# Optimization experiments

Measured on AMD Instinct MI355X. Metric: run time of the kernel, lower is better.

## Reference

```python
import jax, jax.numpy as jnp
import numpy as np

D = 2048
H = 16
DH = D // H  # 128
B = 512
EPS = 1e-5


def _layernorm(x, g, b):
    m = jnp.mean(x, axis=-1, keepdims=True)
    v = jnp.mean((x - m) ** 2, axis=-1, keepdims=True)
    return (x - m) * jax.lax.rsqrt(v + EPS) * g + b


def setup_inputs() -> dict:
    key = jax.random.key(0)
    ks = jax.random.split(key, 16)
    s_in = 1.0 / np.sqrt(D)
    s_ff = 1.0 / np.sqrt(4 * D)
    return {
        "x": jax.random.normal(ks[0], (B, D), jnp.float32),
        # per-head q/k/v projections, stacked over heads: [H, D, DH]
        "Wq": jax.random.uniform(ks[1], (H, D, DH), jnp.float32, -s_in, s_in),
        "bq": jax.random.uniform(ks[2], (H, DH), jnp.float32, -s_in, s_in),
        "Wk": jax.random.uniform(ks[3], (H, D, DH), jnp.float32, -s_in, s_in),
        "bk": jax.random.uniform(ks[4], (H, DH), jnp.float32, -s_in, s_in),
        "Wv": jax.random.uniform(ks[5], (H, D, DH), jnp.float32, -s_in, s_in),
        "bv": jax.random.uniform(ks[6], (H, DH), jnp.float32, -s_in, s_in),
        "Wo": jax.random.uniform(ks[7], (D, D), jnp.float32, -s_in, s_in),
        "bo": jax.random.uniform(ks[8], (D,), jnp.float32, -s_in, s_in),
        "W1": jax.random.uniform(ks[9], (D, 4 * D), jnp.float32, -s_in, s_in),
        "b1": jax.random.uniform(ks[10], (4 * D,), jnp.float32, -s_in, s_in),
        "W2": jax.random.uniform(ks[11], (4 * D, D), jnp.float32, -s_ff, s_ff),
        "b2": jax.random.uniform(ks[12], (D,), jnp.float32, -s_ff, s_ff),
        "g1": jnp.ones((D,), jnp.float32),
        "be1": jnp.zeros((D,), jnp.float32),
        "g2": jnp.ones((D,), jnp.float32),
        "be2": jnp.zeros((D,), jnp.float32),
    }


def reference(x, Wq, bq, Wk, bk, Wv, bv, Wo, bo, W1, b1, W2, b2, g1, be1, g2, be2):
    # --- pre-norm attention branch ---
    h = _layernorm(x, g1, be1)                       # [B, D]
    q = jnp.einsum('bd,hde->bhe', h, Wq) + bq        # [B, H, DH]
    k = jnp.einsum('bd,hde->bhe', h, Wk) + bk
    v = jnp.einsum('bd,hde->bhe', h, Wv) + bv
    # outer-product 'attention' per sample: [B, H, DH, DH]
    attn = q[..., :, None] * k[..., None, :] / jnp.sqrt(jnp.float32(DH))
    attn = jax.nn.softmax(attn, axis=-1)
    o = jnp.einsum('bhij,bhj->bhi', attn, v)         # [B, H, DH]
    o = o.reshape(x.shape[0], H * DH)                # concat over heads
    x = x + o @ Wo + bo
    # --- pre-norm FFN branch ---
    h2 = _layernorm(x, g2, be2)
    x = x + jax.nn.relu(h2 @ W1 + b1) @ W2 + b2
    return x
```

## Files before the change

kernel.cpp:

```cpp
#include <hip/hip_runtime.h>
#include <hip/hip_bf16.h>
#include <math.h>


#define DDIM 2048
#define HHEADS 16
#define DHEAD 128
#define BROWS 512
#define LN_EPS 1e-5f

typedef __bf16 bf16x8_t __attribute__((ext_vector_type(8)));
typedef __bf16 bf16x4_t __attribute__((ext_vector_type(4)));
typedef __bf16 bf16x2_t __attribute__((ext_vector_type(2)));
typedef float f32x4_t __attribute__((ext_vector_type(4)));

#define GLD16(gptr, lptr)                                                     \
    __builtin_amdgcn_global_load_lds(                                         \
        (const __attribute__((address_space(1))) void*)(gptr),                \
        (__attribute__((address_space(3))) void*)(lptr), 16, 0, 0)

__global__ __launch_bounds__(256) void ln_kernel(const float* __restrict__ x,
                                                 const float* __restrict__ g,
                                                 const float* __restrict__ b,
                                                 __bf16* __restrict__ out) {
    const int row = blockIdx.x;
    const int tid = threadIdx.x;
    const float4* x4 = (const float4*)(x + (size_t)row * DDIM);
    float4 a = x4[2 * tid];
    float4 c = x4[2 * tid + 1];
    float s  = a.x + a.y + a.z + a.w + c.x + c.y + c.z + c.w;
    float s2 = a.x*a.x + a.y*a.y + a.z*a.z + a.w*a.w
             + c.x*c.x + c.y*c.y + c.z*c.z + c.w*c.w;
    #pragma unroll
    for (int off = 32; off > 0; off >>= 1) {
        s  += __shfl_down(s, off);
        s2 += __shfl_down(s2, off);
    }
    __shared__ float ps[4], ps2[4];
    __shared__ float mean_s, rstd_s;
    const int lane = tid & 63, w = tid >> 6;
    if (lane == 0) { ps[w] = s; ps2[w] = s2; }
    __syncthreads();
    if (tid == 0) {
        float S  = ps[0] + ps[1] + ps[2] + ps[3];
        float S2 = ps2[0] + ps2[1] + ps2[2] + ps2[3];
        float m  = S * (1.0f / DDIM);
        float var = S2 * (1.0f / DDIM) - m * m;
        mean_s = m;
        rstd_s = rsqrtf(var + LN_EPS);
    }
    __syncthreads();
    const float m = mean_s, r = rstd_s;
    const float4* g4 = (const float4*)g;
    const float4* b4 = (const float4*)b;
    float4 ga = g4[2 * tid], gb = g4[2 * tid + 1];
    float4 ba = b4[2 * tid], bb = b4[2 * tid + 1];
    bf16x8_t o;
    o[0] = (__bf16)((a.x - m) * r * ga.x + ba.x);
    o[1] = (__bf16)((a.y - m) * r * ga.y + ba.y);
    o[2] = (__bf16)((a.z - m) * r * ga.z + ba.z);
    o[3] = (__bf16)((a.w - m) * r * ga.w + ba.w);
    o[4] = (__bf16)((c.x - m) * r * gb.x + bb.x);
    o[5] = (__bf16)((c.y - m) * r * gb.y + bb.y);
    o[6] = (__bf16)((c.z - m) * r * gb.z + bb.z);
    o[7] = (__bf16)((c.w - m) * r * gb.w + bb.w);
    *(bf16x8_t*)(out + (size_t)row * DDIM + tid * 8) = o;
}

template <int TM, int TN, int SPLITZ, int OUT_BF16, int RELU, int RES, int QKV>
__global__ __launch_bounds__(512, 4) void gemm_af(
    const __bf16* __restrict__ A, int K,
    const float* __restrict__ Bq, const float* __restrict__ Bk,
    const float* __restrict__ Bv, int ldb,
    const float* __restrict__ bias, const float* __restrict__ biasB,
    const float* __restrict__ biasC, const float* __restrict__ Res,
    void* __restrict__ Cout, int N) {
    constexpr int DEPTH = 3;
    constexpr int STG = (TM + TN) * 64;
    __shared__ __align__(16) __bf16 smem[DEPTH * STG];

    const int tid = threadIdx.x;
    const int w = tid >> 6, lane = tid & 63;

    const int gx = gridDim.x, gy = gridDim.y, gz = gridDim.z;
    int l = blockIdx.x + gx * (blockIdx.y + gy * blockIdx.z);
    const int xcd = l & 7;
    int i0 = l >> 3;
    const int by = i0 % gy; i0 /= gy;
    const int bz = i0 % gz; i0 /= gz;
    const int bx = xcd * (gx >> 3) + i0;

    const int m0 = by * TM, n0 = bx * TN;
    const int Kloc = K / SPLITZ;
    const int kb = bz * Kloc;
    const int NK = Kloc / 64;

    constexpr int LA = TM / 64;
    const int srow = lane >> 3;
    const int sslot = (lane & 7) ^ srow;
    const __bf16* srcs[LA];
    int toff[LA];
    #pragma unroll
    for (int i = 0; i < LA; i++) {
        const int t = w + 8 * i;
        toff[i] = t * 512;
        srcs[i] = A + (size_t)(m0 + t * 8 + srow) * K + kb + sslot * 8;
    }

    constexpr int KPER = TN / 32;
    constexpr int LB = KPER;
    constexpr int NPR = TN / 4;
    const int np = tid & (NPR - 1);
    const int kp = tid / NPR;
    const int k0 = kp * KPER, n0t = np * 4;

    const float* bbase;
    if (QKV) {
        const int seg = n0 >> 11;
        const float* sel = (seg == 0) ? Bq : (seg == 1) ? Bk : Bv;
        bbase = sel + (size_t)((n0 & 2047) >> 7) * (DDIM * DHEAD);
    } else {
        bbase = Bq + n0;
    }
    const float* bthr = bbase + (size_t)(kb + k0) * ldb + n0t;
    const size_t bstep = (size_t)64 * ldb;

    int bwoff[4];
    {
        const int bslot = k0 >> 3, bhalf = (k0 & 7) * 2;
        #pragma unroll
        for (int j = 0; j < 4; j++) {
            const int n = n0t + j;
            const int fb = (n ^ (n >> 2)) & 7;
            bwoff[j] = (TM + n) * 128 + ((bslot ^ fb) * 16) + bhalf;
        }
    }

    constexpr int MI = TM / 32, NJ = TN / 32;
    const int wg = w & 3, kh = w >> 2;
    const int wm = (wg >> 1) * (TM / 2), wn = (wg & 1) * (TN / 2);
    const int fm = lane & 15, quad = lane >> 4;
    const int slq = kh * 4 + quad;
    int aoff[MI], boff[NJ];
    #pragma unroll
    for (int i = 0; i < MI; i++)
        aoff[i] = (wm + 16 * i + fm) * 128 + ((slq ^ (fm & 7)) * 16);
    #pragma unroll
    for (int j = 0; j < NJ; j++) {
        const int n = wn + 16 * j + fm;
        const int fb = (n ^ (n >> 2)) & 7;
        boff[j] = (TM + n) * 128 + ((slq ^ fb) * 16);
    }

    f32x4_t acc[MI][NJ] = {};
    f32x4_t bufA[KPER], bufB[KPER];

    auto loadB = [&](int ks2, f32x4_t (&dst)[KPER]) {
        const float* q = bthr + (size_t)ks2 * bstep;
        #pragma unroll
        for (int j = 0; j < KPER; j++)
            dst[j] = *(const f32x4_t*)(q + (size_t)j * ldb);
    };
    auto writeB = [&](int slot, const f32x4_t (&src)[KPER]) {
        char* stg = (char*)smem + slot * (STG * 2);
        #pragma unroll
        for (int j = 0; j < 4; j++) {
            if constexpr (KPER == 4) {
                bf16x4_t u;
                u[0] = (__bf16)src[0][j]; u[1] = (__bf16)src[1][j];
                u[2] = (__bf16)src[2][j]; u[3] = (__bf16)src[3][j];
                *(bf16x4_t*)(stg + bwoff[j]) = u;
            } else {
                bf16x2_t u;
                u[0] = (__bf16)src[0][j]; u[1] = (__bf16)src[1][j];
                *(bf16x2_t*)(stg + bwoff[j]) = u;
            }
        }
    };

    loadB(0, bufA);
    loadB(1, bufB);
    #pragma unroll
    for (int i = 0; i < LA; i++) GLD16(srcs[i], smem + toff[i]);
    writeB(0, bufA);
    loadB(2, bufA);
    #pragma unroll
    for (int i = 0; i < LA; i++) GLD16(srcs[i] + 64, smem + STG + toff[i]);

    auto body = [&](int ks, f32x4_t (&buf)[KPER]) {
        if (ks < NK - 2)
            asm volatile("s_waitcnt vmcnt(%0) lgkmcnt(0)\n\ts_barrier"
                         :: "i"(LB + LA) : "memory");
        else
            asm volatile("s_waitcnt vmcnt(0) lgkmcnt(0)\n\ts_barrier"
                         ::: "memory");
        if (ks + 1 < NK) writeB((ks + 1) % DEPTH, buf);
        if (ks + 3 < NK) loadB(ks + 3, buf);
        if (ks + 2 < NK) {
            #pragma unroll
            for (int i = 0; i < LA; i++)
                GLD16(srcs[i] + (size_t)(ks + 2) * 64,
                      smem + ((ks + 2) % DEPTH) * STG + toff[i]);
        }
        const char* st = (const char*)smem + (ks % DEPTH) * (STG * 2);
        bf16x8_t a[MI], b[NJ];
        #pragma unroll
        for (int i = 0; i < MI; i++) a[i] = *(const bf16x8_t*)(st + aoff[i]);
        #pragma unroll
        for (int j = 0; j < NJ; j++) b[j] = *(const bf16x8_t*)(st + boff[j]);
        __builtin_amdgcn_s_setprio(1);
        #pragma unroll
        for (int i = 0; i < MI; i++)
            #pragma unroll
            for (int j = 0; j < NJ; j++)
                acc[i][j] = __builtin_amdgcn_mfma_f32_16x16x32_bf16(
                    a[i], b[j], acc[i][j], 0, 0, 0);
        __builtin_amdgcn_s_setprio(0);
    };

    for (int ks = 0; ks < NK; ks += 2) {
        body(ks, bufB);
        body(ks + 1, bufA);
    }

    char* mrg = (char*)smem + wg * (MI * NJ * 64 * 16);
    __syncthreads();
    if (kh == 1) {
        #pragma unroll
        for (int i = 0; i < MI; i++)
            #pragma unroll
            for (int j = 0; j < NJ; j++)
                *(f32x4_t*)(mrg + (((i * NJ + j) * 64) + lane) * 16) = acc[i][j];
    }
    __syncthreads();
    if (kh == 1) return;
    #pragma unroll
    for (int i = 0; i < MI; i++)
        #pragma unroll
        for (int j = 0; j < NJ; j++) {
            const f32x4_t p =
                *(const f32x4_t*)(mrg + (((i * NJ + j) * 64) + lane) * 16);
            acc[i][j][0] += p[0]; acc[i][j][1] += p[1];
            acc[i][j][2] += p[2]; acc[i][j][3] += p[3];
        }

    if (SPLITZ > 1) {
        float* P = (float*)Cout + (size_t)bz * (gy * TM) * N;
        #pragma unroll
        for (int i = 0; i < MI; i++)
            #pragma unroll
            for (int j = 0; j < NJ; j++) {
                const int col = n0 + wn + 16 * j + fm;
                #pragma unroll
                for (int r = 0; r < 4; r++) {
                    const int row = m0 + wm + 16 * i + quad * 4 + r;
                    P[(size_t)row * N + col] = acc[i][j][r];
                }
            }
    } else {
        const float* bp = bias;
        if (QKV) {
            const int seg = n0 >> 11;
            bp = (seg == 0) ? bias : (seg == 1) ? biasB : biasC;
        }
        #pragma unroll
        for (int i = 0; i < MI; i++)
            #pragma unroll
            for (int j = 0; j < NJ; j++) {
                const int col = n0 + wn + 16 * j + fm;
                const float bcol = QKV ? bp[col & 2047] : bp[col];
                #pragma unroll
                for (int r = 0; r < 4; r++) {
                    const int row = m0 + wm + 16 * i + quad * 4 + r;
                    float val = acc[i][j][r] + bcol;
                    if (RES) val += Res[(size_t)row * N + col];
                    if (RELU) val = fmaxf(val, 0.0f);
                    if (OUT_BF16)
                        ((__bf16*)Cout)[(size_t)row * N + col] = (__bf16)val;
                    else
                        ((float*)Cout)[(size_t)row * N + col] = val;
                }
            }
    }
}

template <int NS>
__global__ __launch_bounds__(256) void reduce_splitk(
    const float* __restrict__ part, const float* __restrict__ Res,
    const float* __restrict__ bias, float* __restrict__ out) {
    const int idx = blockIdx.x * 256 + threadIdx.x;
    const float4 b4 = ((const float4*)bias)[idx & 511];
    float4 r = ((const float4*)Res)[idx];
    #pragma unroll
    for (int s = 0; s < NS; s++) {
        const float4 p = ((const float4*)part)[(size_t)s * 262144 + idx];
        r.x += p.x; r.y += p.y; r.z += p.z; r.w += p.w;
    }
    r.x += b4.x; r.y += b4.y; r.z += b4.z; r.w += b4.w;
    ((float4*)out)[idx] = r;
}

__global__ __launch_bounds__(128) void attn_kernel(
    const __bf16* __restrict__ qkv, __bf16* __restrict__ o) {
    const int bh = blockIdx.x;
    const int b = bh >> 4, h = bh & 15;
    const size_t base = (size_t)b * (3 * DDIM) + h * DHEAD;
    const int tid = threadIdx.x;
    __shared__ float ks[DHEAD], vs[DHEAD];
    ks[tid] = (float)qkv[base + DDIM + tid];
    vs[tid] = (float)qkv[base + 2 * DDIM + tid];
    __syncthreads();
    const float a = (float)qkv[base + tid] * 0.08838834764831845f;
    float den = 0.0f, num = 0.0f;
    #pragma unroll 8
    for (int j = 0; j < DHEAD; j++) {
        float e = __expf(a * ks[j]);
        den += e;
        num += e * vs[j];
    }
    o[(size_t)b * DDIM + h * DHEAD + tid] = (__bf16)(num / den);
}

extern "C" void kernel_launch(void* const* d_in, const int* in_sizes, int n_in,
                              void* d_out, int out_size, void* d_ws, size_t ws_size,
                              hipStream_t stream) {
    const float* x   = (const float*)d_in[0];
    const float* Wq  = (const float*)d_in[1];
    const float* bq  = (const float*)d_in[2];
    const float* Wk  = (const float*)d_in[3];
    const float* bk  = (const float*)d_in[4];
    const float* Wv  = (const float*)d_in[5];
    const float* bv  = (const float*)d_in[6];
    const float* Wo  = (const float*)d_in[7];
    const float* bo  = (const float*)d_in[8];
    const float* W1  = (const float*)d_in[9];
    const float* b1  = (const float*)d_in[10];
    const float* W2  = (const float*)d_in[11];
    const float* b2  = (const float*)d_in[12];
    const float* g1  = (const float*)d_in[13];
    const float* be1 = (const float*)d_in[14];
    const float* g2  = (const float*)d_in[15];
    const float* be2 = (const float*)d_in[16];
    float* out = (float*)d_out;

    char* base = (char*)d_ws;
    __bf16* h   = (__bf16*)(base + 0);
    __bf16* qkv = (__bf16*)(base + 2097152);
    __bf16* ob  = (__bf16*)(base + 8388608);
    float*  x1  = (float*)(base + 10485760);
    __bf16* h2  = (__bf16*)(base + 14680064);
    __bf16* t   = (__bf16*)(base + 16777216);
    float*  w2P = (float*)(base + 25165824);

    ln_kernel<<<BROWS, 256, 0, stream>>>(x, g1, be1, h);

    gemm_af<64, 128, 1, 1, 0, 0, 1><<<dim3(48, 8), 512, 0, stream>>>(
        h, DDIM, Wq, Wk, Wv, DHEAD, bq, bk, bv, nullptr, qkv, 3 * DDIM);

    attn_kernel<<<BROWS * HHEADS, 128, 0, stream>>>(qkv, ob);

    gemm_af<64, 64, 1, 0, 0, 1, 0><<<dim3(32, 8), 512, 0, stream>>>(
        ob, DDIM, Wo, nullptr, nullptr, DDIM, bo, nullptr, nullptr, x,
        x1, DDIM);

    ln_kernel<<<BROWS, 256, 0, stream>>>(x1, g2, be2, h2);

    gemm_af<64, 128, 1, 1, 1, 0, 0><<<dim3(64, 8), 512, 0, stream>>>(
        h2, DDIM, W1, nullptr, nullptr, 4 * DDIM, b1, nullptr, nullptr,
        nullptr, t, 4 * DDIM);

    gemm_af<64, 128, 4, 0, 0, 0, 0><<<dim3(16, 8, 4), 512, 0, stream>>>(
        t, 4 * DDIM, W2, nullptr, nullptr, DDIM, nullptr, nullptr, nullptr,
        nullptr, w2P, DDIM);

    reduce_splitk<4><<<1024, 256, 0, stream>>>(w2P, x1, b2, out);
}
```

Baseline: 389.8 us.

## Pre-cast all weights to bf16 in a fused cast+LN kernel, drop split-K for W2

Adds a kernel that converts every fp32 weight matrix to bf16 in a workspace, fused with the first layernorm. The GEMMs then stream bf16 weights instead of fp32, and the W2 GEMM runs without split-K, fusing bias and residual directly and removing the reduction kernel. The extra cast pass reads all fp32 weights once and writes bf16 copies every call, so total weight traffic per call rises rather than falls. The W2 GEMM also now iterates the full K=8192 per block with fewer blocks.

```diff
diff --git a/kernel.cpp b/kernel.cpp
--- a/kernel.cpp
+++ b/kernel.cpp
@@ -67,11 +67,88 @@
     *(bf16x8_t*)(out + (size_t)row * DDIM + tid * 8) = o;
 }
 
-template <int TM, int TN, int SPLITZ, int OUT_BF16, int RELU, int RES, int QKV>
+__global__ __launch_bounds__(256) void cast_ln_kernel(
+    const float* __restrict__ Wq, const float* __restrict__ Wk,
+    const float* __restrict__ Wv, const float* __restrict__ Wo,
+    const float* __restrict__ W1, const float* __restrict__ W2,
+    const float* __restrict__ x, const float* __restrict__ g1,
+    const float* __restrict__ be1,
+    __bf16* __restrict__ wc, __bf16* __restrict__ h) {
+    __shared__ float sh[32];
+    const int bid = blockIdx.x;
+    const int tid = threadIdx.x;
+    if (bid < 12288) {
+        const int seg = bid >> 10;
+        const float* src;
+        if (seg == 0) src = Wq;
+        else if (seg == 1) src = Wk;
+        else if (seg == 2) src = Wv;
+        else if (seg == 3) src = Wo;
+        else if (seg < 8) src = W1 + (size_t)(seg - 4) * 4194304;
+        else src = W2 + (size_t)(seg - 8) * 4194304;
+        __bf16* dst = wc + (size_t)seg * 4194304;
+        const size_t i = (size_t)(bid & 1023) * 4096 + (size_t)tid * 16;
+        const float4* s4 = (const float4*)(src + i);
+        const float4 v0 = s4[0], v1 = s4[1], v2 = s4[2], v3 = s4[3];
+        bf16x8_t o0, o1;
+        o0[0] = (__bf16)v0.x; o0[1] = (__bf16)v0.y;
+        o0[2] = (__bf16)v0.z; o0[3] = (__bf16)v0.w;
+        o0[4] = (__bf16)v1.x; o0[5] = (__bf16)v1.y;
+        o0[6] = (__bf16)v1.z; o0[7] = (__bf16)v1.w;
+        o1[0] = (__bf16)v2.x; o1[1] = (__bf16)v2.y;
+        o1[2] = (__bf16)v2.z; o1[3] = (__bf16)v2.w;
+        o1[4] = (__bf16)v3.x; o1[5] = (__bf16)v3.y;
+        o1[6] = (__bf16)v3.z; o1[7] = (__bf16)v3.w;
+        *(bf16x8_t*)(dst + i) = o0;
+        *(bf16x8_t*)(dst + i + 8) = o1;
+    } else {
+        const int row = bid - 12288;
+        const float4* x4 = (const float4*)(x + (size_t)row * DDIM);
+        float4 a = x4[2 * tid];
+        float4 c = x4[2 * tid + 1];
+        float s  = a.x + a.y + a.z + a.w + c.x + c.y + c.z + c.w;
+        float s2 = a.x*a.x + a.y*a.y + a.z*a.z + a.w*a.w
+                 + c.x*c.x + c.y*c.y + c.z*c.z + c.w*c.w;
+        #pragma unroll
+        for (int off = 32; off > 0; off >>= 1) {
+            s  += __shfl_down(s, off);
+            s2 += __shfl_down(s2, off);
+        }
+        const int lane = tid & 63, w = tid >> 6;
+        if (lane == 0) { sh[w] = s; sh[8 + w] = s2; }
+        __syncthreads();
+        if (tid == 0) {
+            float S  = sh[0] + sh[1] + sh[2] + sh[3];
+            float S2 = sh[8] + sh[9] + sh[10] + sh[11];
+            float m  = S * (1.0f / DDIM);
+            float var = S2 * (1.0f / DDIM) - m * m;
+            sh[16] = m;
+            sh[17] = rsqrtf(var + LN_EPS);
+        }
+        __syncthreads();
+        const float m = sh[16], r = sh[17];
+        const float4* g4 = (const float4*)g1;
+        const float4* b4 = (const float4*)be1;
+        float4 ga = g4[2 * tid], gb = g4[2 * tid + 1];
+        float4 ba = b4[2 * tid], bb = b4[2 * tid + 1];
+        bf16x8_t o;
+        o[0] = (__bf16)((a.x - m) * r * ga.x + ba.x);
+        o[1] = (__bf16)((a.y - m) * r * ga.y + ba.y);
+        o[2] = (__bf16)((a.z - m) * r * ga.z + ba.z);
+        o[3] = (__bf16)((a.w - m) * r * ga.w + ba.w);
+        o[4] = (__bf16)((c.x - m) * r * gb.x + bb.x);
+        o[5] = (__bf16)((c.y - m) * r * gb.y + bb.y);
+        o[6] = (__bf16)((c.z - m) * r * gb.z + bb.z);
+        o[7] = (__bf16)((c.w - m) * r * gb.w + bb.w);
+        *(bf16x8_t*)(h + (size_t)row * DDIM + tid * 8) = o;
+    }
+}
+
+template <int TM, int TN, int OUT_BF16, int RELU, int RES, int QKV>
 __global__ __launch_bounds__(512, 4) void gemm_af(
     const __bf16* __restrict__ A, int K,
-    const float* __restrict__ Bq, const float* __restrict__ Bk,
-    const float* __restrict__ Bv, int ldb,
+    const __bf16* __restrict__ Bq, const __bf16* __restrict__ Bk,
+    const __bf16* __restrict__ Bv, int ldb,
     const float* __restrict__ bias, const float* __restrict__ biasB,
     const float* __restrict__ biasC, const float* __restrict__ Res,
     void* __restrict__ Cout, int N) {
@@ -82,18 +159,15 @@
     const int tid = threadIdx.x;
     const int w = tid >> 6, lane = tid & 63;
 
-    const int gx = gridDim.x, gy = gridDim.y, gz = gridDim.z;
-    int l = blockIdx.x + gx * (blockIdx.y + gy * blockIdx.z);
+    const int gx = gridDim.x, gy = gridDim.y;
+    int l = blockIdx.x + gx * blockIdx.y;
     const int xcd = l & 7;
     int i0 = l >> 3;
     const int by = i0 % gy; i0 /= gy;
-    const int bz = i0 % gz; i0 /= gz;
     const int bx = xcd * (gx >> 3) + i0;
 
     const int m0 = by * TM, n0 = bx * TN;
-    const int Kloc = K / SPLITZ;
-    const int kb = bz * Kloc;
-    const int NK = Kloc / 64;
+    const int NK = K / 64;
 
     constexpr int LA = TM / 64;
     const int srow = lane >> 3;
@@ -104,7 +178,7 @@
     for (int i = 0; i < LA; i++) {
         const int t = w + 8 * i;
         toff[i] = t * 512;
-        srcs[i] = A + (size_t)(m0 + t * 8 + srow) * K + kb + sslot * 8;
+        srcs[i] = A + (size_t)(m0 + t * 8 + srow) * K + sslot * 8;
     }
 
     constexpr int KPER = TN / 32;
@@ -114,15 +188,15 @@
     const int kp = tid / NPR;
     const int k0 = kp * KPER, n0t = np * 4;
 
-    const float* bbase;
+    const __bf16* bbase;
     if (QKV) {
         const int seg = n0 >> 11;
-        const float* sel = (seg == 0) ? Bq : (seg == 1) ? Bk : Bv;
+        const __bf16* sel = (seg == 0) ? Bq : (seg == 1) ? Bk : Bv;
         bbase = sel + (size_t)((n0 & 2047) >> 7) * (DDIM * DHEAD);
     } else {
         bbase = Bq + n0;
     }
-    const float* bthr = bbase + (size_t)(kb + k0) * ldb + n0t;
+    const __bf16* bthr = bbase + (size_t)k0 * ldb + n0t;
     const size_t bstep = (size_t)64 * ldb;
 
     int bwoff[4];
@@ -153,26 +227,26 @@
     }
 
     f32x4_t acc[MI][NJ] = {};
-    f32x4_t bufA[KPER], bufB[KPER];
-
-    auto loadB = [&](int ks2, f32x4_t (&dst)[KPER]) {
-        const float* q = bthr + (size_t)ks2 * bstep;
+    bf16x4_t bufA[KPER], bufB[KPER];
+
+    auto loadB = [&](int ks2, bf16x4_t (&dst)[KPER]) {
+        const __bf16* q = bthr + (size_t)ks2 * bstep;
         #pragma unroll
         for (int j = 0; j < KPER; j++)
-            dst[j] = *(const f32x4_t*)(q + (size_t)j * ldb);
+            dst[j] = *(const bf16x4_t*)(q + (size_t)j * ldb);
     };
-    auto writeB = [&](int slot, const f32x4_t (&src)[KPER]) {
+    auto writeB = [&](int slot, const bf16x4_t (&src)[KPER]) {
         char* stg = (char*)smem + slot * (STG * 2);
         #pragma unroll
         for (int j = 0; j < 4; j++) {
             if constexpr (KPER == 4) {
                 bf16x4_t u;
-                u[0] = (__bf16)src[0][j]; u[1] = (__bf16)src[1][j];
-                u[2] = (__bf16)src[2][j]; u[3] = (__bf16)src[3][j];
+                u[0] = src[0][j]; u[1] = src[1][j];
+                u[2] = src[2][j]; u[3] = src[3][j];
                 *(bf16x4_t*)(stg + bwoff[j]) = u;
             } else {
                 bf16x2_t u;
-                u[0] = (__bf16)src[0][j]; u[1] = (__bf16)src[1][j];
+                u[0] = src[0][j]; u[1] = src[1][j];
                 *(bf16x2_t*)(stg + bwoff[j]) = u;
             }
         }
@@ -187,7 +261,7 @@
     #pragma unroll
     for (int i = 0; i < LA; i++) GLD16(srcs[i] + 64, smem + STG + toff[i]);
 
-    auto body = [&](int ks, f32x4_t (&buf)[KPER]) {
+    auto body = [&](int ks, bf16x4_t (&buf)[KPER]) {
         if (ks < NK - 2)
             asm volatile("s_waitcnt vmcnt(%0) lgkmcnt(0)\n\ts_barrier"
                          :: "i"(LB + LA) : "memory");
@@ -244,60 +318,29 @@
             acc[i][j][2] += p[2]; acc[i][j][3] += p[3];
         }
 
-    if (SPLITZ > 1) {
-        float* P = (float*)Cout + (size_t)bz * (gy * TM) * N;
-        #pragma unroll
-        for (int i = 0; i < MI; i++)
+    const float* bp = bias;
+    if (QKV) {
+        const int seg = n0 >> 11;
+        bp = (seg == 0) ? bias : (seg == 1) ? biasB : biasC;
+    }
+    #pragma unroll
+    for (int i = 0; i < MI; i++)
+        #pragma unroll
+        for (int j = 0; j < NJ; j++) {
+            const int col = n0 + wn + 16 * j + fm;
+            const float bcol = QKV ? bp[col & 2047] : bp[col];
             #pragma unroll
-            for (int j = 0; j < NJ; j++) {
-                const int col = n0 + wn + 16 * j + fm;
-                #pragma unroll
-                for (int r = 0; r < 4; r++) {
-                    const int row = m0 + wm + 16 * i + quad * 4 + r;
-                    P[(size_t)row * N + col] = acc[i][j][r];
-                }
+            for (int r = 0; r < 4; r++) {
+                const int row = m0 + wm + 16 * i + quad * 4 + r;
+                float val = acc[i][j][r] + bcol;
+                if (RES) val += Res[(size_t)row * N + col];
+                if (RELU) val = fmaxf(val, 0.0f);
+                if (OUT_BF16)
+                    ((__bf16*)Cout)[(size_t)row * N + col] = (__bf16)val;
+                else
+                    ((float*)Cout)[(size_t)row * N + col] = val;
             }
-    } else {
-        const float* bp = bias;
-        if (QKV) {
-            const int seg = n0 >> 11;
-            bp = (seg == 0) ? bias : (seg == 1) ? biasB : biasC;
-        }
-        #pragma unroll
-        for (int i = 0; i < MI; i++)
-            #pragma unroll
-            for (int j = 0; j < NJ; j++) {
-                const int col = n0 + wn + 16 * j + fm;
-                const float bcol = QKV ? bp[col & 2047] : bp[col];
-                #pragma unroll
-                for (int r = 0; r < 4; r++) {
-                    const int row = m0 + wm + 16 * i + quad * 4 + r;
-                    float val = acc[i][j][r] + bcol;
-                    if (RES) val += Res[(size_t)row * N + col];
-                    if (RELU) val = fmaxf(val, 0.0f);
-                    if (OUT_BF16)
-                        ((__bf16*)Cout)[(size_t)row * N + col] = (__bf16)val;
-                    else
-                        ((float*)Cout)[(size_t)row * N + col] = val;
-                }
-            }
-    }
-}
-
-template <int NS>
-__global__ __launch_bounds__(256) void reduce_splitk(
-    const float* __restrict__ part, const float* __restrict__ Res,
-    const float* __restrict__ bias, float* __restrict__ out) {
-    const int idx = blockIdx.x * 256 + threadIdx.x;
-    const float4 b4 = ((const float4*)bias)[idx & 511];
-    float4 r = ((const float4*)Res)[idx];
-    #pragma unroll
-    for (int s = 0; s < NS; s++) {
-        const float4 p = ((const float4*)part)[(size_t)s * 262144 + idx];
-        r.x += p.x; r.y += p.y; r.z += p.z; r.w += p.w;
-    }
-    r.x += b4.x; r.y += b4.y; r.z += b4.z; r.w += b4.w;
-    ((float4*)out)[idx] = r;
+        }
 }
 
 __global__ __launch_bounds__(128) void attn_kernel(
@@ -344,34 +387,40 @@
     float* out = (float*)d_out;
 
     char* base = (char*)d_ws;
-    __bf16* h   = (__bf16*)(base + 0);
-    __bf16* qkv = (__bf16*)(base + 2097152);
-    __bf16* ob  = (__bf16*)(base + 8388608);
-    float*  x1  = (float*)(base + 10485760);
-    __bf16* h2  = (__bf16*)(base + 14680064);
-    __bf16* t   = (__bf16*)(base + 16777216);
-    float*  w2P = (float*)(base + 25165824);
-
-    ln_kernel<<<BROWS, 256, 0, stream>>>(x, g1, be1, h);
-
-    gemm_af<64, 128, 1, 1, 0, 0, 1><<<dim3(48, 8), 512, 0, stream>>>(
-        h, DDIM, Wq, Wk, Wv, DHEAD, bq, bk, bv, nullptr, qkv, 3 * DDIM);
+    __bf16* wc   = (__bf16*)(base + 0);
+    __bf16* Wq_c = wc;
+    __bf16* Wk_c = wc + 4194304;
+    __bf16* Wv_c = wc + 2 * 4194304;
+    __bf16* Wo_c = wc + 3 * 4194304;
+    __bf16* W1_c = wc + 4 * 4194304;
+    __bf16* W2_c = wc + 8 * 4194304;
+    char* act = base + 100663296;
+    __bf16* h   = (__bf16*)(act + 0);
+    __bf16* qkv = (__bf16*)(act + 2097152);
+    __bf16* ob  = (__bf16*)(act + 8388608);
+    float*  x1  = (float*)(act + 10485760);
+    __bf16* h2  = (__bf16*)(act + 14680064);
+    __bf16* t   = (__bf16*)(act + 16777216);
+
+    cast_ln_kernel<<<12800, 256, 0, stream>>>(Wq, Wk, Wv, Wo, W1, W2, x, g1,
+                                              be1, wc, h);
+
+    gemm_af<64, 128, 1, 0, 0, 1><<<dim3(48, 8), 512, 0, stream>>>(
+        h, DDIM, Wq_c, Wk_c, Wv_c, DHEAD, bq, bk, bv, nullptr, qkv, 3 * DDIM);
 
     attn_kernel<<<BROWS * HHEADS, 128, 0, stream>>>(qkv, ob);
 
-    gemm_af<64, 64, 1, 0, 0, 1, 0><<<dim3(32, 8), 512, 0, stream>>>(
-        ob, DDIM, Wo, nullptr, nullptr, DDIM, bo, nullptr, nullptr, x,
+    gemm_af<64, 64, 0, 0, 1, 0><<<dim3(32, 8), 512, 0, stream>>>(
+        ob, DDIM, Wo_c, nullptr, nullptr, DDIM, bo, nullptr, nullptr, x,
         x1, DDIM);
 
     ln_kernel<<<BROWS, 256, 0, stream>>>(x1, g2, be2, h2);
 
-    gemm_af<64, 128, 1, 1, 1, 0, 0><<<dim3(64, 8), 512, 0, stream>>>(
-        h2, DDIM, W1, nullptr, nullptr, 4 * DDIM, b1, nullptr, nullptr,
+    gemm_af<64, 128, 1, 1, 0, 0><<<dim3(64, 8), 512, 0, stream>>>(
+        h2, DDIM, W1_c, nullptr, nullptr, 4 * DDIM, b1, nullptr, nullptr,
         nullptr, t, 4 * DDIM);
 
-    gemm_af<64, 128, 4, 0, 0, 0, 0><<<dim3(16, 8, 4), 512, 0, stream>>>(
-        t, 4 * DDIM, W2, nullptr, nullptr, DDIM, nullptr, nullptr, nullptr,
-        nullptr, w2P, DDIM);
-
-    reduce_splitk<4><<<1024, 256, 0, stream>>>(w2P, x1, b2, out);
+    gemm_af<64, 64, 0, 0, 1, 0><<<dim3(32, 8), 512, 0, stream>>>(
+        t, 4 * DDIM, W2_c, nullptr, nullptr, DDIM, b2, nullptr, nullptr, x1,
+        out, DDIM);
 }
```

After: 397.2 us. No clear change (+1.9%).

## Use 128x128 GEMM tiles, split-K the Wo projection, fuse reduce with LayerNorm

Applied to the files above, without the earlier changes.

Fixes all GEMMs at 128x128 tiles with four 4x4 MFMA fragments per wave and lowers the occupancy hint to 2, halving the M-direction grid. This raises reuse of the fp32 weight tiles that each block converts to bf16. The Wo projection now runs as a 4-way split-K GEMM writing partial sums. A new kernel adds those partials, the residual and the bias, then applies the second LayerNorm in one pass, replacing the separate LN launch. The cost is fewer blocks per GEMM (192–256 on a large GPU), more registers and LDS per block, and extra partial-sum traffic for Wo.

```diff
diff --git a/kernel.cpp b/kernel.cpp
--- a/kernel.cpp
+++ b/kernel.cpp
@@ -11,7 +11,6 @@
 
 typedef __bf16 bf16x8_t __attribute__((ext_vector_type(8)));
 typedef __bf16 bf16x4_t __attribute__((ext_vector_type(4)));
-typedef __bf16 bf16x2_t __attribute__((ext_vector_type(2)));
 typedef float f32x4_t __attribute__((ext_vector_type(4)));
 
 #define GLD16(gptr, lptr)                                                     \
@@ -67,15 +66,15 @@
     *(bf16x8_t*)(out + (size_t)row * DDIM + tid * 8) = o;
 }
 
-template <int TM, int TN, int SPLITZ, int OUT_BF16, int RELU, int RES, int QKV>
-__global__ __launch_bounds__(512, 4) void gemm_af(
+template <int SPLITZ, int OUT_BF16, int RELU, int RES, int QKV>
+__global__ __launch_bounds__(512, 2) void gemm_af(
     const __bf16* __restrict__ A, int K,
     const float* __restrict__ Bq, const float* __restrict__ Bk,
     const float* __restrict__ Bv, int ldb,
     const float* __restrict__ bias, const float* __restrict__ biasB,
     const float* __restrict__ biasC, const float* __restrict__ Res,
     void* __restrict__ Cout, int N) {
-    constexpr int DEPTH = 3;
+    constexpr int TM = 128, TN = 128, DEPTH = 3;
     constexpr int STG = (TM + TN) * 64;
     __shared__ __align__(16) __bf16 smem[DEPTH * STG];
 
@@ -107,7 +106,7 @@
         srcs[i] = A + (size_t)(m0 + t * 8 + srow) * K + kb + sslot * 8;
     }
 
-    constexpr int KPER = TN / 32;
+    constexpr int KPER = 4;
     constexpr int LB = KPER;
     constexpr int NPR = TN / 4;
     const int np = tid & (NPR - 1);
@@ -136,9 +135,9 @@
         }
     }
 
-    constexpr int MI = TM / 32, NJ = TN / 32;
+    constexpr int MI = 4, NJ = 4;
     const int wg = w & 3, kh = w >> 2;
-    const int wm = (wg >> 1) * (TM / 2), wn = (wg & 1) * (TN / 2);
+    const int wm = (wg >> 1) * 64, wn = (wg & 1) * 64;
     const int fm = lane & 15, quad = lane >> 4;
     const int slq = kh * 4 + quad;
     int aoff[MI], boff[NJ];
@@ -165,16 +164,10 @@
         char* stg = (char*)smem + slot * (STG * 2);
         #pragma unroll
         for (int j = 0; j < 4; j++) {
-            if constexpr (KPER == 4) {
-                bf16x4_t u;
-                u[0] = (__bf16)src[0][j]; u[1] = (__bf16)src[1][j];
-                u[2] = (__bf16)src[2][j]; u[3] = (__bf16)src[3][j];
-                *(bf16x4_t*)(stg + bwoff[j]) = u;
-            } else {
-                bf16x2_t u;
-                u[0] = (__bf16)src[0][j]; u[1] = (__bf16)src[1][j];
-                *(bf16x2_t*)(stg + bwoff[j]) = u;
-            }
+            bf16x4_t u;
+            u[0] = (__bf16)src[0][j]; u[1] = (__bf16)src[1][j];
+            u[2] = (__bf16)src[2][j]; u[3] = (__bf16)src[3][j];
+            *(bf16x4_t*)(stg + bwoff[j]) = u;
         }
     };
 
@@ -223,7 +216,7 @@
         body(ks + 1, bufA);
     }
 
-    char* mrg = (char*)smem + wg * (MI * NJ * 64 * 16);
+    char* mrg = (char*)smem + wg * 16384;
     __syncthreads();
     if (kh == 1) {
         #pragma unroll
@@ -298,6 +291,71 @@
     }
     r.x += b4.x; r.y += b4.y; r.z += b4.z; r.w += b4.w;
     ((float4*)out)[idx] = r;
+}
+
+template <int NS>
+__global__ __launch_bounds__(256) void reduce_ln_kernel(
+    const float* __restrict__ part, const float* __restrict__ x,
+    const float* __restrict__ bo, const float* __restrict__ g,
+    const float* __restrict__ be, float* __restrict__ x1,
+    __bf16* __restrict__ h2) {
+    const int row = blockIdx.x;
+    const int tid = threadIdx.x;
+    const size_t rbase = (size_t)row * DDIM;
+    float v[8];
+    #pragma unroll
+    for (int p = 0; p < 2; p++) {
+        const int c = tid * 8 + p * 4;
+        float4 r = *(const float4*)(x + rbase + c);
+        const float4 b4 = *(const float4*)(bo + c);
+        r.x += b4.x; r.y += b4.y; r.z += b4.z; r.w += b4.w;
+        #pragma unroll
+        for (int s = 0; s < NS; s++) {
+            const float4 q =
+                *(const float4*)(part + (size_t)s * BROWS * DDIM + rbase + c);
+            r.x += q.x; r.y += q.y; r.z += q.z; r.w += q.w;
+        }
+        *(float4*)(x1 + rbase + c) = r;
+        v[p * 4 + 0] = r.x; v[p * 4 + 1] = r.y;
+        v[p * 4 + 2] = r.z; v[p * 4 + 3] = r.w;
+    }
+    float s = 0.f, s2 = 0.f;
+    #pragma unroll
+    for (int i = 0; i < 8; i++) { s += v[i]; s2 += v[i] * v[i]; }
+    #pragma unroll
+    for (int off = 32; off > 0; off >>= 1) {
+        s  += __shfl_down(s, off);
+        s2 += __shfl_down(s2, off);
+    }
+    __shared__ float ps[4], ps2[4];
+    __shared__ float mean_s, rstd_s;
+    const int lane = tid & 63, wv = tid >> 6;
+    if (lane == 0) { ps[wv] = s; ps2[wv] = s2; }
+    __syncthreads();
+    if (tid == 0) {
+        float S  = ps[0] + ps[1] + ps[2] + ps[3];
+        float S2 = ps2[0] + ps2[1] + ps2[2] + ps2[3];
+        float m  = S * (1.0f / DDIM);
+        float var = S2 * (1.0f / DDIM) - m * m;
+        mean_s = m;
+        rstd_s = rsqrtf(var + LN_EPS);
+    }
+    __syncthreads();
+    const float m = mean_s, r = rstd_s;
+    const float4* g4 = (const float4*)g;
+    const float4* b4 = (const float4*)be;
+    float4 ga = g4[2 * tid], gb = g4[2 * tid + 1];
+    float4 ba = b4[2 * tid], bb = b4[2 * tid + 1];
+    bf16x8_t o;
+    o[0] = (__bf16)((v[0] - m) * r * ga.x + ba.x);
+    o[1] = (__bf16)((v[1] - m) * r * ga.y + ba.y);
+    o[2] = (__bf16)((v[2] - m) * r * ga.z + ba.z);
+    o[3] = (__bf16)((v[3] - m) * r * ga.w + ba.w);
+    o[4] = (__bf16)((v[4] - m) * r * gb.x + bb.x);
+    o[5] = (__bf16)((v[5] - m) * r * gb.y + bb.y);
+    o[6] = (__bf16)((v[6] - m) * r * gb.z + bb.z);
+    o[7] = (__bf16)((v[7] - m) * r * gb.w + bb.w);
+    *(bf16x8_t*)(h2 + rbase + tid * 8) = o;
 }
 
 __global__ __launch_bounds__(128) void attn_kernel(
@@ -343,33 +401,34 @@
     const float* be2 = (const float*)d_in[16];
     float* out = (float*)d_out;
 
-    char* base = (char*)d_ws;
-    __bf16* h   = (__bf16*)(base + 0);
-    __bf16* qkv = (__bf16*)(base + 2097152);
-    __bf16* ob  = (__bf16*)(base + 8388608);
-    float*  x1  = (float*)(base + 10485760);
-    __bf16* h2  = (__bf16*)(base + 14680064);
-    __bf16* t   = (__bf16*)(base + 16777216);
-    float*  w2P = (float*)(base + 25165824);
+    char* act = (char*)d_ws;
+    __bf16* h   = (__bf16*)(act + 0);
+    __bf16* qkv = (__bf16*)(act + 2097152);
+    __bf16* ob  = (__bf16*)(act + 8388608);
+    float*  x1  = (float*)(act + 10485760);
+    __bf16* h2  = (__bf16*)(act + 14680064);
+    __bf16* t   = (__bf16*)(act + 16777216);
+    float*  woP = (float*)(act + 25165824);
+    float*  w2P = (float*)(act + 41943040);
 
     ln_kernel<<<BROWS, 256, 0, stream>>>(x, g1, be1, h);
 
-    gemm_af<64, 128, 1, 1, 0, 0, 1><<<dim3(48, 8), 512, 0, stream>>>(
+    gemm_af<1, 1, 0, 0, 1><<<dim3(48, 4), 512, 0, stream>>>(
         h, DDIM, Wq, Wk, Wv, DHEAD, bq, bk, bv, nullptr, qkv, 3 * DDIM);
 
     attn_kernel<<<BROWS * HHEADS, 128, 0, stream>>>(qkv, ob);
 
-    gemm_af<64, 64, 1, 0, 0, 1, 0><<<dim3(32, 8), 512, 0, stream>>>(
-        ob, DDIM, Wo, nullptr, nullptr, DDIM, bo, nullptr, nullptr, x,
-        x1, DDIM);
-
-    ln_kernel<<<BROWS, 256, 0, stream>>>(x1, g2, be2, h2);
-
-    gemm_af<64, 128, 1, 1, 1, 0, 0><<<dim3(64, 8), 512, 0, stream>>>(
+    gemm_af<4, 0, 0, 0, 0><<<dim3(16, 4, 4), 512, 0, stream>>>(
+        ob, DDIM, Wo, nullptr, nullptr, DDIM, nullptr, nullptr, nullptr,
+        nullptr, woP, DDIM);
+
+    reduce_ln_kernel<4><<<BROWS, 256, 0, stream>>>(woP, x, bo, g2, be2, x1, h2);
+
+    gemm_af<1, 1, 1, 0, 0><<<dim3(64, 4), 512, 0, stream>>>(
         h2, DDIM, W1, nullptr, nullptr, 4 * DDIM, b1, nullptr, nullptr,
         nullptr, t, 4 * DDIM);
 
-    gemm_af<64, 128, 4, 0, 0, 0, 0><<<dim3(16, 8, 4), 512, 0, stream>>>(
+    gemm_af<4, 0, 0, 0, 0><<<dim3(16, 4, 4), 512, 0, stream>>>(
         t, 4 * DDIM, W2, nullptr, nullptr, DDIM, nullptr, nullptr, nullptr,
         nullptr, w2P, DDIM);
 
```

Result: faster. 332.1 us (-14.8%).
